# Kernel optimization log

Hardware: AMD Instinct MI355X
Metric: run time of the kernel (lower is better)

Reference implementation:

```python
import jax, jax.numpy as jnp
import numpy as np

B, T, C, UNITS = 64, 1000, 320, 320


def _lstm_scan(x_tbc, m_tb, W, U, b):
    """Masked LSTM over leading time axis.
    x_tbc: [T,B,C], m_tb: [T,B] bool. Keras gate order i,f,c(g),o.
    Masked steps carry (h,c) through unchanged and emit the carried h,
    matching Keras masking semantics. Returns (ys [T,B,U], h_T [B,U]).
    """
    units = U.shape[0]
    h0 = jnp.zeros((x_tbc.shape[1], units), x_tbc.dtype)

    def step(carry, inp):
        h, c = carry
        xt, mt = inp
        z = xt @ W + h @ U + b                      # [B, 4U]
        i, f, g, o = jnp.split(z, 4, axis=-1)
        i = jax.nn.sigmoid(i)
        f = jax.nn.sigmoid(f)
        g = jnp.tanh(g)
        o = jax.nn.sigmoid(o)
        c_new = f * c + i * g
        h_new = o * jnp.tanh(c_new)
        mt = mt[:, None]
        h = jnp.where(mt, h_new, h)
        c = jnp.where(mt, c_new, c)
        return (h, c), h

    (hT, cT), ys = jax.lax.scan(step, (h0, h0), (x_tbc, m_tb))
    return ys, hT


def setup_inputs() -> dict:
    key = jax.random.key(0)
    ks = jax.random.split(key, 8)
    inputs = jax.random.normal(ks[0], (B, T, C), dtype=jnp.float32)
    # padding mask: variable sequence lengths in [T//2, T]
    seq_len = jax.random.randint(ks[1], (B,), T // 2, T + 1)
    mask = (jnp.arange(T)[None, :] < seq_len[:, None])  # [B, T] bool
    s_in = 1.0 / np.sqrt(C)
    s_rec = 1.0 / np.sqrt(UNITS)
    W_fwd = jax.random.normal(ks[2], (C, 4 * UNITS), jnp.float32) * s_in
    U_fwd = jax.random.normal(ks[3], (UNITS, 4 * UNITS), jnp.float32) * s_rec
    b_fwd = jnp.zeros((4 * UNITS,), jnp.float32).at[UNITS:2 * UNITS].set(1.0)  # unit forget bias
    W_bwd = jax.random.normal(ks[4], (C, 4 * UNITS), jnp.float32) * s_in
    U_bwd = jax.random.normal(ks[5], (UNITS, 4 * UNITS), jnp.float32) * s_rec
    b_bwd = jnp.zeros((4 * UNITS,), jnp.float32).at[UNITS:2 * UNITS].set(1.0)
    return {"inputs": inputs, "mask": mask, "W_fwd": W_fwd, "U_fwd": U_fwd,
            "b_fwd": b_fwd, "W_bwd": W_bwd, "U_bwd": U_bwd, "b_bwd": b_bwd}


def reference(inputs, mask, W_fwd, U_fwd, b_fwd, W_bwd, U_bwd, b_bwd):
    x = jnp.transpose(inputs, (1, 0, 2))   # [T,B,C]
    m = jnp.transpose(mask, (1, 0))        # [T,B]
    # forward direction
    ys_f, h_f = _lstm_scan(x, m, W_fwd, U_fwd, b_fwd)
    # backward direction: go_backwards reverses time; Bidirectional flips output back
    ys_b, h_b = _lstm_scan(x[::-1], m[::-1], W_bwd, U_bwd, b_bwd)
    ys_b = ys_b[::-1]
    sequence_output = jnp.transpose(jnp.concatenate([ys_f, ys_b], axis=-1), (1, 0, 2))  # [B,T,2U]
    state_output = jnp.concatenate([h_f, h_b], axis=-1)  # [B,2U]
    return sequence_output, state_output
```

## Files before the change

kernel.cpp:

```cpp
#include <hip/hip_runtime.h>
#include <hip/hip_bf16.h>
#include <stdint.h>


#define Bx 64
#define Tx 1000
#define Cx 320
#define NSLICE 20
#define UPW 16
#define SENT 0xFFFFFFFFFFFFFFFFull

typedef __attribute__((ext_vector_type(8))) short short8;
typedef __attribute__((ext_vector_type(4))) short short4v;
typedef __attribute__((ext_vector_type(4))) float f32x4;

__device__ inline unsigned short f2bf(float f) {
  unsigned x = __builtin_bit_cast(unsigned, f);
  x += 0x7fffu + ((x >> 16) & 1u);
  return (unsigned short)(x >> 16);
}
__device__ inline float bf2f(unsigned short u) {
  unsigned x = ((unsigned)u) << 16;
  return __builtin_bit_cast(float, x);
}

#define OFF_MB   0ull
#define OFF_HB   16384ull
#define OFF_XB   0ull
#define OFF_WT   40960000ull
#define OFF_BP   42598400ull
#define OFF_ZX   42608640ull

__global__ __launch_bounds__(256) void k_prep_x(const float* __restrict__ X,
                                                unsigned short* __restrict__ Xb) {
  int i4 = blockIdx.x * 256 + threadIdx.x;
  if (i4 >= Bx * Tx * Cx / 4) return;
  int idx = i4 * 4;
  int b = idx / (Tx * Cx);
  int rem = idx - b * (Tx * Cx);
  int t = rem / Cx;
  int c = rem - t * Cx;
  float4 v = *(const float4*)(X + idx);
  short4v o;
  o[0] = (short)f2bf(v.x); o[1] = (short)f2bf(v.y);
  o[2] = (short)f2bf(v.z); o[3] = (short)f2bf(v.w);
  *(short4v*)(Xb + (size_t)(t * Bx + b) * Cx + c) = o;
}

__global__ __launch_bounds__(256) void k_prep_w(const float* __restrict__ Wf,
                                                const float* __restrict__ Wb,
                                                const float* __restrict__ bfv,
                                                const float* __restrict__ bbv,
                                                unsigned short* __restrict__ Wt,
                                                float* __restrict__ biasp) {
  int gid = blockIdx.x * 256 + threadIdx.x;
  if (gid < 2 * 1280 * 320) {
    int dir = gid / (1280 * 320);
    int rem = gid - dir * 1280 * 320;
    int n = rem / 320;
    int k = rem - n * 320;
    int u = n >> 2, g = n & 3;
    const float* W = dir ? Wb : Wf;
    Wt[gid] = f2bf(W[k * 1280 + g * 320 + u]);
  }
  if (gid < 2 * 1280) {
    int dir = gid / 1280, n = gid - dir * 1280;
    int u = n >> 2, g = n & 3;
    const float* bsrc = dir ? bbv : bfv;
    biasp[gid] = bsrc[g * 320 + u];
  }
}

__global__ __launch_bounds__(256) void k_prep_mask(const void* __restrict__ maskp,
                                                   unsigned long long* __restrict__ mask2) {
  int t = blockIdx.x * 256 + threadIdx.x;
  if (t >= Tx) return;
  const unsigned* mw = (const unsigned*)maskp;
  const bool mbyte = (mw[0] == 0x01010101u);
  unsigned long long wv = 0ull;
  if (mbyte) {
    const unsigned char* m8 = (const unsigned char*)maskp;
#pragma unroll 8
    for (int b = 0; b < Bx; b++)
      wv |= (unsigned long long)(m8[b * Tx + t] & 1) << b;
  } else {
    const int* m32 = (const int*)maskp;
#pragma unroll 8
    for (int b = 0; b < Bx; b++)
      wv |= (unsigned long long)(m32[b * Tx + t] & 1) << b;
  }
  mask2[t] = wv;
}

__global__ __launch_bounds__(256) void k_gemm(const unsigned short* __restrict__ A,
                                              const unsigned short* __restrict__ Bt,
                                              const float* __restrict__ biasp,
                                              unsigned short* __restrict__ Czx) {
  int bid = blockIdx.x;
  int dir = bid / 5000;
  int r = bid - dir * 5000;
  int tm = r / 10, tn = r - (r / 10) * 10;
  long m0 = (long)tm * 128;
  int n0 = tn * 128;
  const unsigned short* Bd = Bt + (size_t)dir * 1280 * 320;
  const float* bias = biasp + dir * 1280;

  __shared__ __align__(16) unsigned short As[128 * 64];
  __shared__ __align__(16) unsigned short Bs[128 * 64];

  int tid = threadIdx.x;
  int wave = tid >> 6, lane = tid & 63;
  int l15 = lane & 15, l4 = lane >> 4;

  f32x4 acc[2][8];
#pragma unroll
  for (int i = 0; i < 2; i++)
#pragma unroll
    for (int j = 0; j < 8; j++) acc[i][j] = (f32x4){0.f, 0.f, 0.f, 0.f};

  for (int k0 = 0; k0 < 320; k0 += 64) {
    __syncthreads();
#pragma unroll
    for (int it = 0; it < 4; it++) {
      int idx = it * 256 + tid;
      int rr = idx >> 3, cc = idx & 7;
      const unsigned short* ga = A + (size_t)(m0 + rr) * 320 + k0 + cc * 8;
      unsigned short* la = As + (size_t)(it * 256 + wave * 64) * 8;
      __builtin_amdgcn_global_load_lds(
          (const __attribute__((address_space(1))) void*)ga,
          (__attribute__((address_space(3))) void*)la, 16, 0, 0);
      const unsigned short* gb = Bd + (size_t)(n0 + rr) * 320 + k0 + cc * 8;
      unsigned short* lb = Bs + (size_t)(it * 256 + wave * 64) * 8;
      __builtin_amdgcn_global_load_lds(
          (const __attribute__((address_space(1))) void*)gb,
          (__attribute__((address_space(3))) void*)lb, 16, 0, 0);
    }
    __syncthreads();
#pragma unroll
    for (int kk = 0; kk < 2; kk++) {
      short8 af[2], bf8[8];
#pragma unroll
      for (int mf = 0; mf < 2; mf++)
        af[mf] = *(const short8*)(As + (wave * 32 + mf * 16 + l15) * 64 + kk * 32 + l4 * 8);
#pragma unroll
      for (int nf = 0; nf < 8; nf++)
        bf8[nf] = *(const short8*)(Bs + (nf * 16 + l15) * 64 + kk * 32 + l4 * 8);
#pragma unroll
      for (int mf = 0; mf < 2; mf++)
#pragma unroll
        for (int nf = 0; nf < 8; nf++)
          acc[mf][nf] = __builtin_amdgcn_mfma_f32_16x16x32_bf16(af[mf], bf8[nf], acc[mf][nf], 0, 0, 0);
    }
  }
#pragma unroll
  for (int mf = 0; mf < 2; mf++) {
#pragma unroll
    for (int nf = 0; nf < 8; nf++) {
      int col = n0 + nf * 16 + l15;
      float bv = bias[col];
      int slice = col >> 6, i64v = col & 63;
      size_t sbase = ((size_t)(dir * NSLICE + slice)) * Tx * 4096;
#pragma unroll
      for (int i = 0; i < 4; i++) {
        long m = m0 + wave * 32 + mf * 16 + l4 * 4 + i;
        long t = m >> 6;
        int b = (int)(m & 63);
        Czx[sbase + (size_t)t * 4096 + b * 64 + i64v] = f2bf(acc[mf][nf][i] + bv);
      }
    }
  }
}

__global__ __launch_bounds__(256, 1) void k_lstm(const unsigned short* __restrict__ Zx,
                                                 const float* __restrict__ Uf,
                                                 const float* __restrict__ Ub,
                                                 const unsigned long long* __restrict__ mask2,
                                                 unsigned short* __restrict__ hring,
                                                 float* __restrict__ out) {
  const int w = blockIdx.x;
  const int dir = w / NSLICE;
  const int slice = w - dir * NSLICE;
  const int u0 = slice * UPW;
  const int tid = threadIdx.x;
  const int wave = tid >> 6, lane = tid & 63;
  const int l15 = lane & 15, l4 = lane >> 4;

  const float* U = dir ? Ub : Uf;
  short8 bfrag[4][10];
#pragma unroll
  for (int nf = 0; nf < 4; nf++) {
    int ncol = nf * 16 + l15;
    int colU = (ncol & 3) * 320 + u0 + (ncol >> 2);
#pragma unroll
    for (int kt = 0; kt < 10; kt++) {
      short8 v;
#pragma unroll
      for (int j = 0; j < 8; j++)
        v[j] = (short)f2bf(U[(size_t)(kt * 32 + l4 * 8 + j) * 1280 + colU]);
      bfrag[nf][kt] = v;
    }
  }

  const int pb = tid >> 2;
  const int uq = tid & 3;
  const int arow = wave * 16 + l15;
  float c0 = 0.f, c1 = 0.f, c2 = 0.f, c3 = 0.f;
  float h0 = 0.f, h1 = 0.f, h2 = 0.f, h3 = 0.f;

  __shared__ float zsh[64][68];

  const unsigned short* zbase = Zx + ((size_t)(dir * NSLICE + slice)) * Tx * 4096;
#define HR(SL) (hring + ((size_t)((SL) * 2 + dir)) * Bx * 320)

  int t = dir ? (Tx - 1) : 0;
  short8 zv0 = *(const short8*)(zbase + (size_t)t * 4096 + pb * 64 + uq * 16);
  short8 zv1 = *(const short8*)(zbase + (size_t)t * 4096 + pb * 64 + uq * 16 + 8);
  unsigned long long mwrd = mask2[t];

  unsigned long long q[20];
  const unsigned long long* pollp = nullptr;

  for (int s = 0;; ++s) {
    t = dir ? (Tx - 1 - s) : s;
    float4 zr0, zr1, zr2, zr3;
    if (s > 0) {
      for (;;) {
        bool any = false;
#pragma unroll
        for (int i = 0; i < 20; i++) any |= (q[i] == SENT);
        if (!any) break;
#pragma unroll
        for (int i = 0; i < 20; i++)
          if (q[i] == SENT)
            q[i] = __hip_atomic_load(pollp + (i >> 1) * 8 + (i & 1),
                                     __ATOMIC_RELAXED, __HIP_MEMORY_SCOPE_AGENT);
      }
      short8 afr[10];
#pragma unroll
      for (int kt = 0; kt < 10; kt++) {
        union { unsigned long long qq[2]; short8 v; } u;
        u.qq[0] = q[2 * kt];
        u.qq[1] = q[2 * kt + 1];
        afr[kt] = u.v;
      }
#pragma unroll
      for (int nf = 0; nf < 4; nf++) {
        f32x4 a0 = {0.f, 0.f, 0.f, 0.f}, a1 = {0.f, 0.f, 0.f, 0.f};
#pragma unroll
        for (int k2 = 0; k2 < 5; k2++) {
          a0 = __builtin_amdgcn_mfma_f32_16x16x32_bf16(afr[2 * k2], bfrag[nf][2 * k2], a0, 0, 0, 0);
          a1 = __builtin_amdgcn_mfma_f32_16x16x32_bf16(afr[2 * k2 + 1], bfrag[nf][2 * k2 + 1], a1, 0, 0, 0);
        }
        int rr = wave * 16 + l4 * 4;
        zsh[rr + 0][nf * 16 + l15] = a0[0] + a1[0];
        zsh[rr + 1][nf * 16 + l15] = a0[1] + a1[1];
        zsh[rr + 2][nf * 16 + l15] = a0[2] + a1[2];
        zsh[rr + 3][nf * 16 + l15] = a0[3] + a1[3];
      }
      __syncthreads();
      zr0 = *(const float4*)&zsh[pb][uq * 16 + 0];
      zr1 = *(const float4*)&zsh[pb][uq * 16 + 4];
      zr2 = *(const float4*)&zsh[pb][uq * 16 + 8];
      zr3 = *(const float4*)&zsh[pb][uq * 16 + 12];
    } else {
      zr0 = zr1 = zr2 = zr3 = make_float4(0.f, 0.f, 0.f, 0.f);
    }

    int mv = (int)((mwrd >> pb) & 1ull);
#define GATES(CC, HH, Z0, Z1, Z2, Z3, ZR)                              \
    {                                                                  \
      float zi = bf2f((unsigned short)(Z0)) + (ZR).x;                  \
      float zf = bf2f((unsigned short)(Z1)) + (ZR).y;                  \
      float zg = bf2f((unsigned short)(Z2)) + (ZR).z;                  \
      float zo = bf2f((unsigned short)(Z3)) + (ZR).w;                  \
      float ig = 1.f / (1.f + __expf(-zi));                            \
      float fg = 1.f / (1.f + __expf(-zf));                            \
      float gg = 2.f / (1.f + __expf(-2.f * zg)) - 1.f;                \
      float og = 1.f / (1.f + __expf(-zo));                            \
      float cn = fg * (CC) + ig * gg;                                  \
      float hn = og * (2.f / (1.f + __expf(-2.f * cn)) - 1.f);         \
      if (mv) { (CC) = cn; (HH) = hn; }                                \
    }
    GATES(c0, h0, zv0[0], zv0[1], zv0[2], zv0[3], zr0)
    GATES(c1, h1, zv0[4], zv0[5], zv0[6], zv0[7], zr1)
    GATES(c2, h2, zv1[0], zv1[1], zv1[2], zv1[3], zr2)
    GATES(c3, h3, zv1[4], zv1[5], zv1[6], zv1[7], zr3)
#undef GATES

    union { float f[4]; unsigned long long qq[2]; } ou;
    ou.f[0] = h0; ou.f[1] = h1; ou.f[2] = h2; ou.f[3] = h3;

    if (s < Tx - 1) {
      unsigned long long hv =
          (unsigned long long)f2bf(h0) | ((unsigned long long)f2bf(h1) << 16) |
          ((unsigned long long)f2bf(h2) << 32) | ((unsigned long long)f2bf(h3) << 48);
      __hip_atomic_store((unsigned long long*)(HR(s & 3) + pb * 320 + u0 + uq * 4),
                         hv, __ATOMIC_RELAXED, __HIP_MEMORY_SCOPE_AGENT);
    }

    unsigned long long* op = (unsigned long long*)(out +
        ((size_t)pb * Tx + t) * 640 + dir * 320 + u0 + uq * 4);
    __hip_atomic_store(op, ou.qq[0], __ATOMIC_RELAXED, __HIP_MEMORY_SCOPE_AGENT);
    __hip_atomic_store(op + 1, ou.qq[1], __ATOMIC_RELAXED, __HIP_MEMORY_SCOPE_AGENT);
    if (s == Tx - 1) {
      unsigned long long* fp = (unsigned long long*)(out + 40960000ull +
          (size_t)pb * 640 + dir * 320 + u0 + uq * 4);
      __hip_atomic_store(fp, ou.qq[0], __ATOMIC_RELAXED, __HIP_MEMORY_SCOPE_AGENT);
      __hip_atomic_store(fp + 1, ou.qq[1], __ATOMIC_RELAXED, __HIP_MEMORY_SCOPE_AGENT);
      break;
    }

    __hip_atomic_store((unsigned long long*)(HR((s + 2) & 3) + pb * 320 + u0 + uq * 4),
                       SENT, __ATOMIC_RELAXED, __HIP_MEMORY_SCOPE_AGENT);

    int tn = dir ? (Tx - 2 - s) : (s + 1);
    zv0 = *(const short8*)(zbase + (size_t)tn * 4096 + pb * 64 + uq * 16);
    zv1 = *(const short8*)(zbase + (size_t)tn * 4096 + pb * 64 + uq * 16 + 8);
    mwrd = mask2[tn];

    pollp = (const unsigned long long*)(HR(s & 3) + arow * 320 + l4 * 8);
#pragma unroll
    for (int i = 0; i < 20; i++)
      q[i] = __hip_atomic_load(pollp + (i >> 1) * 8 + (i & 1),
                               __ATOMIC_RELAXED, __HIP_MEMORY_SCOPE_AGENT);
  }
#undef HR
}

extern "C" void kernel_launch(void* const* d_in, const int* in_sizes, int n_in,
                              void* d_out, int out_size, void* d_ws, size_t ws_size,
                              hipStream_t stream) {
  const float* X = (const float*)d_in[0];
  const void* Mk = d_in[1];
  const float* Wf = (const float*)d_in[2];
  const float* Uf = (const float*)d_in[3];
  const float* bfv = (const float*)d_in[4];
  const float* Wb = (const float*)d_in[5];
  const float* Ub = (const float*)d_in[6];
  const float* bbv = (const float*)d_in[7];

  char* ws = (char*)d_ws;
  unsigned short* Xb = (unsigned short*)(ws + OFF_XB);
  unsigned short* Wt = (unsigned short*)(ws + OFF_WT);
  float* bp = (float*)(ws + OFF_BP);
  unsigned short* Zx = (unsigned short*)(ws + OFF_ZX);
  unsigned long long* mask2 = (unsigned long long*)(ws + OFF_MB);
  unsigned short* hring = (unsigned short*)(ws + OFF_HB);

  k_prep_x<<<dim3(20000), dim3(256), 0, stream>>>(X, Xb);
  k_prep_w<<<dim3(3200), dim3(256), 0, stream>>>(Wf, Wb, bfv, bbv, Wt, bp);
  k_gemm<<<dim3(10000), dim3(256), 0, stream>>>(Xb, Wt, bp, Zx);
  hipMemsetAsync(ws + OFF_HB, 0xFF, 327680, stream);
  k_prep_mask<<<dim3(4), dim3(256), 0, stream>>>(Mk, mask2);
  k_lstm<<<dim3(2 * NSLICE), dim3(256), 0, stream>>>(Zx, Uf, Ub, mask2, hring,
                                                     (float*)d_out);
}
```

Measured before the change: 5.295 ms.

## Swap MFMA operands so gates land in registers, dropping LDS round-trip and barrier

The Zx column layout and the recurrent weight fragments are reordered so each gate (i,f,g,o) gets its own accumulator. The MFMA operands are swapped (U as A, h as B), so each lane ends up holding all four gate pre-activations for its batch row and units. This removes the per-step shared-memory transpose and the __syncthreads on the serial critical path. It also adds a spin-limit escape in the poll loop, an explicit vmcnt wait, and plain vector stores for the output, at the risk of subtle ordering or correctness problems in the permuted K layout of the h ring.

```diff
diff --git a/kernel.cpp b/kernel.cpp
--- a/kernel.cpp
+++ b/kernel.cpp
@@ -59,15 +59,13 @@
     int rem = gid - dir * 1280 * 320;
     int n = rem / 320;
     int k = rem - n * 320;
-    int u = n >> 2, g = n & 3;
     const float* W = dir ? Wb : Wf;
-    Wt[gid] = f2bf(W[k * 1280 + g * 320 + u]);
+    Wt[gid] = f2bf(W[k * 1280 + n]);
   }
   if (gid < 2 * 1280) {
     int dir = gid / 1280, n = gid - dir * 1280;
-    int u = n >> 2, g = n & 3;
     const float* bsrc = dir ? bbv : bfv;
-    biasp[gid] = bsrc[g * 320 + u];
+    biasp[gid] = bsrc[n];
   }
 }
 
@@ -158,14 +156,17 @@
     for (int nf = 0; nf < 8; nf++) {
       int col = n0 + nf * 16 + l15;
       float bv = bias[col];
-      int slice = col >> 6, i64v = col & 63;
-      size_t sbase = ((size_t)(dir * NSLICE + slice)) * Tx * 4096;
+      int g = col / 320;
+      int u = col - g * 320;
+      int sl = u >> 4;
+      int cp = g * 16 + (u & 15);
+      size_t sbase = ((size_t)(dir * NSLICE + sl)) * Tx * 4096;
 #pragma unroll
       for (int i = 0; i < 4; i++) {
         long m = m0 + wave * 32 + mf * 16 + l4 * 4 + i;
         long t = m >> 6;
         int b = (int)(m & 63);
-        Czx[sbase + (size_t)t * 4096 + b * 64 + i64v] = f2bf(acc[mf][nf][i] + bv);
+        Czx[sbase + (size_t)t * 4096 + b * 64 + cp] = f2bf(acc[mf][nf][i] + bv);
       }
     }
   }
@@ -183,57 +184,58 @@
   const int u0 = slice * UPW;
   const int tid = threadIdx.x;
   const int wave = tid >> 6, lane = tid & 63;
-  const int l15 = lane & 15, l4 = lane >> 4;
+  const int l15 = lane & 15, q4 = lane >> 4;
 
   const float* U = dir ? Ub : Uf;
   short8 bfrag[4][10];
 #pragma unroll
-  for (int nf = 0; nf < 4; nf++) {
-    int ncol = nf * 16 + l15;
-    int colU = (ncol & 3) * 320 + u0 + (ncol >> 2);
+  for (int g = 0; g < 4; g++) {
+    int colU = g * 320 + u0 + l15;
 #pragma unroll
     for (int kt = 0; kt < 10; kt++) {
       short8 v;
 #pragma unroll
       for (int j = 0; j < 8; j++)
-        v[j] = (short)f2bf(U[(size_t)(kt * 32 + l4 * 8 + j) * 1280 + colU]);
-      bfrag[nf][kt] = v;
-    }
-  }
-
-  const int pb = tid >> 2;
-  const int uq = tid & 3;
-  const int arow = wave * 16 + l15;
-  float c0 = 0.f, c1 = 0.f, c2 = 0.f, c3 = 0.f;
-  float h0 = 0.f, h1 = 0.f, h2 = 0.f, h3 = 0.f;
-
-  __shared__ float zsh[64][68];
+        v[j] = (short)f2bf(U[(size_t)(kt * 32 + q4 * 8 + j) * 1280 + colU]);
+      bfrag[g][kt] = v;
+    }
+  }
+
+  const int b = 16 * wave + l15;
+  float cst0 = 0.f, cst1 = 0.f, cst2 = 0.f, cst3 = 0.f;
+  float hst0 = 0.f, hst1 = 0.f, hst2 = 0.f, hst3 = 0.f;
 
   const unsigned short* zbase = Zx + ((size_t)(dir * NSLICE + slice)) * Tx * 4096;
 #define HR(SL) (hring + ((size_t)((SL) * 2 + dir)) * Bx * 320)
 
   int t = dir ? (Tx - 1) : 0;
-  short8 zv0 = *(const short8*)(zbase + (size_t)t * 4096 + pb * 64 + uq * 16);
-  short8 zv1 = *(const short8*)(zbase + (size_t)t * 4096 + pb * 64 + uq * 16 + 8);
+  unsigned long long zx0 = *(const unsigned long long*)(zbase + (size_t)t * 4096 + b * 64 + 0 * 16 + 4 * q4);
+  unsigned long long zx1 = *(const unsigned long long*)(zbase + (size_t)t * 4096 + b * 64 + 1 * 16 + 4 * q4);
+  unsigned long long zx2 = *(const unsigned long long*)(zbase + (size_t)t * 4096 + b * 64 + 2 * 16 + 4 * q4);
+  unsigned long long zx3 = *(const unsigned long long*)(zbase + (size_t)t * 4096 + b * 64 + 3 * 16 + 4 * q4);
   unsigned long long mwrd = mask2[t];
 
   unsigned long long q[20];
-  const unsigned long long* pollp = nullptr;
+  const unsigned short* pollb = nullptr;
 
   for (int s = 0;; ++s) {
     t = dir ? (Tx - 1 - s) : s;
-    float4 zr0, zr1, zr2, zr3;
+    f32x4 acc0 = {0.f, 0.f, 0.f, 0.f}, acc1 = {0.f, 0.f, 0.f, 0.f};
+    f32x4 acc2 = {0.f, 0.f, 0.f, 0.f}, acc3 = {0.f, 0.f, 0.f, 0.f};
     if (s > 0) {
+      unsigned spin = 0;
       for (;;) {
         bool any = false;
 #pragma unroll
         for (int i = 0; i < 20; i++) any |= (q[i] == SENT);
         if (!any) break;
+        if (++spin > 65536u) break;
 #pragma unroll
         for (int i = 0; i < 20; i++)
           if (q[i] == SENT)
-            q[i] = __hip_atomic_load(pollp + (i >> 1) * 8 + (i & 1),
-                                     __ATOMIC_RELAXED, __HIP_MEMORY_SCOPE_AGENT);
+            q[i] = __hip_atomic_load(
+                (const unsigned long long*)(pollb + (i >> 1) * 32 + q4 * 8 + (i & 1) * 4),
+                __ATOMIC_RELAXED, __HIP_MEMORY_SCOPE_AGENT);
       }
       short8 afr[10];
 #pragma unroll
@@ -244,35 +246,25 @@
         afr[kt] = u.v;
       }
 #pragma unroll
-      for (int nf = 0; nf < 4; nf++) {
-        f32x4 a0 = {0.f, 0.f, 0.f, 0.f}, a1 = {0.f, 0.f, 0.f, 0.f};
-#pragma unroll
-        for (int k2 = 0; k2 < 5; k2++) {
-          a0 = __builtin_amdgcn_mfma_f32_16x16x32_bf16(afr[2 * k2], bfrag[nf][2 * k2], a0, 0, 0, 0);
-          a1 = __builtin_amdgcn_mfma_f32_16x16x32_bf16(afr[2 * k2 + 1], bfrag[nf][2 * k2 + 1], a1, 0, 0, 0);
-        }
-        int rr = wave * 16 + l4 * 4;
-        zsh[rr + 0][nf * 16 + l15] = a0[0] + a1[0];
-        zsh[rr + 1][nf * 16 + l15] = a0[1] + a1[1];
-        zsh[rr + 2][nf * 16 + l15] = a0[2] + a1[2];
-        zsh[rr + 3][nf * 16 + l15] = a0[3] + a1[3];
+      for (int k2 = 0; k2 < 5; k2++) {
+        acc0 = __builtin_amdgcn_mfma_f32_16x16x32_bf16(bfrag[0][2 * k2], afr[2 * k2], acc0, 0, 0, 0);
+        acc1 = __builtin_amdgcn_mfma_f32_16x16x32_bf16(bfrag[1][2 * k2], afr[2 * k2], acc1, 0, 0, 0);
+        acc2 = __builtin_amdgcn_mfma_f32_16x16x32_bf16(bfrag[2][2 * k2], afr[2 * k2], acc2, 0, 0, 0);
+        acc3 = __builtin_amdgcn_mfma_f32_16x16x32_bf16(bfrag[3][2 * k2], afr[2 * k2], acc3, 0, 0, 0);
+        acc0 = __builtin_amdgcn_mfma_f32_16x16x32_bf16(bfrag[0][2 * k2 + 1], afr[2 * k2 + 1], acc0, 0, 0, 0);
+        acc1 = __builtin_amdgcn_mfma_f32_16x16x32_bf16(bfrag[1][2 * k2 + 1], afr[2 * k2 + 1], acc1, 0, 0, 0);
+        acc2 = __builtin_amdgcn_mfma_f32_16x16x32_bf16(bfrag[2][2 * k2 + 1], afr[2 * k2 + 1], acc2, 0, 0, 0);
+        acc3 = __builtin_amdgcn_mfma_f32_16x16x32_bf16(bfrag[3][2 * k2 + 1], afr[2 * k2 + 1], acc3, 0, 0, 0);
       }
-      __syncthreads();
-      zr0 = *(const float4*)&zsh[pb][uq * 16 + 0];
-      zr1 = *(const float4*)&zsh[pb][uq * 16 + 4];
-      zr2 = *(const float4*)&zsh[pb][uq * 16 + 8];
-      zr3 = *(const float4*)&zsh[pb][uq * 16 + 12];
-    } else {
-      zr0 = zr1 = zr2 = zr3 = make_float4(0.f, 0.f, 0.f, 0.f);
-    }
-
-    int mv = (int)((mwrd >> pb) & 1ull);
-#define GATES(CC, HH, Z0, Z1, Z2, Z3, ZR)                              \
+    }
+
+    int mv = (int)((mwrd >> b) & 1ull);
+#define GATES(R, CC, HH)                                               \
     {                                                                  \
-      float zi = bf2f((unsigned short)(Z0)) + (ZR).x;                  \
-      float zf = bf2f((unsigned short)(Z1)) + (ZR).y;                  \
-      float zg = bf2f((unsigned short)(Z2)) + (ZR).z;                  \
-      float zo = bf2f((unsigned short)(Z3)) + (ZR).w;                  \
+      float zi = acc0[R] + bf2f((unsigned short)(zx0 >> (16 * R)));    \
+      float zf = acc1[R] + bf2f((unsigned short)(zx1 >> (16 * R)));    \
+      float zg = acc2[R] + bf2f((unsigned short)(zx2 >> (16 * R)));    \
+      float zo = acc3[R] + bf2f((unsigned short)(zx3 >> (16 * R)));    \
       float ig = 1.f / (1.f + __expf(-zi));                            \
       float fg = 1.f / (1.f + __expf(-zf));                            \
       float gg = 2.f / (1.f + __expf(-2.f * zg)) - 1.f;                \
@@ -281,48 +273,45 @@
       float hn = og * (2.f / (1.f + __expf(-2.f * cn)) - 1.f);         \
       if (mv) { (CC) = cn; (HH) = hn; }                                \
     }
-    GATES(c0, h0, zv0[0], zv0[1], zv0[2], zv0[3], zr0)
-    GATES(c1, h1, zv0[4], zv0[5], zv0[6], zv0[7], zr1)
-    GATES(c2, h2, zv1[0], zv1[1], zv1[2], zv1[3], zr2)
-    GATES(c3, h3, zv1[4], zv1[5], zv1[6], zv1[7], zr3)
+    GATES(0, cst0, hst0)
+    GATES(1, cst1, hst1)
+    GATES(2, cst2, hst2)
+    GATES(3, cst3, hst3)
 #undef GATES
 
-    union { float f[4]; unsigned long long qq[2]; } ou;
-    ou.f[0] = h0; ou.f[1] = h1; ou.f[2] = h2; ou.f[3] = h3;
+    asm volatile("s_waitcnt vmcnt(0)" ::: "memory");
 
     if (s < Tx - 1) {
       unsigned long long hv =
-          (unsigned long long)f2bf(h0) | ((unsigned long long)f2bf(h1) << 16) |
-          ((unsigned long long)f2bf(h2) << 32) | ((unsigned long long)f2bf(h3) << 48);
-      __hip_atomic_store((unsigned long long*)(HR(s & 3) + pb * 320 + u0 + uq * 4),
+          (unsigned long long)f2bf(hst0) | ((unsigned long long)f2bf(hst1) << 16) |
+          ((unsigned long long)f2bf(hst2) << 32) | ((unsigned long long)f2bf(hst3) << 48);
+      __hip_atomic_store((unsigned long long*)(HR(s & 3) + b * 320 + u0 + 4 * q4),
                          hv, __ATOMIC_RELAXED, __HIP_MEMORY_SCOPE_AGENT);
     }
 
-    unsigned long long* op = (unsigned long long*)(out +
-        ((size_t)pb * Tx + t) * 640 + dir * 320 + u0 + uq * 4);
-    __hip_atomic_store(op, ou.qq[0], __ATOMIC_RELAXED, __HIP_MEMORY_SCOPE_AGENT);
-    __hip_atomic_store(op + 1, ou.qq[1], __ATOMIC_RELAXED, __HIP_MEMORY_SCOPE_AGENT);
+    float4 ov = make_float4(hst0, hst1, hst2, hst3);
+    *(float4*)(out + ((size_t)b * Tx + t) * 640 + dir * 320 + u0 + 4 * q4) = ov;
     if (s == Tx - 1) {
-      unsigned long long* fp = (unsigned long long*)(out + 40960000ull +
-          (size_t)pb * 640 + dir * 320 + u0 + uq * 4);
-      __hip_atomic_store(fp, ou.qq[0], __ATOMIC_RELAXED, __HIP_MEMORY_SCOPE_AGENT);
-      __hip_atomic_store(fp + 1, ou.qq[1], __ATOMIC_RELAXED, __HIP_MEMORY_SCOPE_AGENT);
+      *(float4*)(out + 40960000ull + (size_t)b * 640 + dir * 320 + u0 + 4 * q4) = ov;
       break;
     }
 
-    __hip_atomic_store((unsigned long long*)(HR((s + 2) & 3) + pb * 320 + u0 + uq * 4),
+    __hip_atomic_store((unsigned long long*)(HR((s + 2) & 3) + b * 320 + u0 + 4 * q4),
                        SENT, __ATOMIC_RELAXED, __HIP_MEMORY_SCOPE_AGENT);
 
     int tn = dir ? (Tx - 2 - s) : (s + 1);
-    zv0 = *(const short8*)(zbase + (size_t)tn * 4096 + pb * 64 + uq * 16);
-    zv1 = *(const short8*)(zbase + (size_t)tn * 4096 + pb * 64 + uq * 16 + 8);
+    zx0 = *(const unsigned long long*)(zbase + (size_t)tn * 4096 + b * 64 + 0 * 16 + 4 * q4);
+    zx1 = *(const unsigned long long*)(zbase + (size_t)tn * 4096 + b * 64 + 1 * 16 + 4 * q4);
+    zx2 = *(const unsigned long long*)(zbase + (size_t)tn * 4096 + b * 64 + 2 * 16 + 4 * q4);
+    zx3 = *(const unsigned long long*)(zbase + (size_t)tn * 4096 + b * 64 + 3 * 16 + 4 * q4);
     mwrd = mask2[tn];
 
-    pollp = (const unsigned long long*)(HR(s & 3) + arow * 320 + l4 * 8);
+    pollb = HR(s & 3) + b * 320;
 #pragma unroll
     for (int i = 0; i < 20; i++)
-      q[i] = __hip_atomic_load(pollp + (i >> 1) * 8 + (i & 1),
-                               __ATOMIC_RELAXED, __HIP_MEMORY_SCOPE_AGENT);
+      q[i] = __hip_atomic_load(
+          (const unsigned long long*)(pollb + (i >> 1) * 32 + q4 * 8 + (i & 1) * 4),
+          __ATOMIC_RELAXED, __HIP_MEMORY_SCOPE_AGENT);
   }
 #undef HR
 }
```

Measured after the change: 5.385 ms. Within noise of the previous version (+1.7%).
